# Optimization experiments

Hardware: AMD Instinct MI355X
Metric: run time of the kernel (lower is better)

## Reference

```python
import jax, jax.numpy as jnp
import numpy as np

NUM_HEADS, KEY_DIM, BLOCK, HALO = 8, 64, 8, 4
KV_KERNEL = BLOCK + 2 * HALO  # 16
EMB = NUM_HEADS * KEY_DIM     # 512


def setup_inputs() -> dict:
    key = jax.random.key(0)
    k = jax.random.split(key, 6)
    stddev = KEY_DIM ** -0.5
    return {
        "x": jax.random.normal(k[0], (8, 64, 64, 512), jnp.float32),
        "wq": jax.random.normal(k[1], (512, EMB), jnp.float32) * 0.02,
        "wkv": jax.random.normal(k[2], (512, 2 * EMB), jnp.float32) * 0.02,
        "wout": jax.random.normal(k[3], (EMB, EMB), jnp.float32) * 0.02,
        "pos_w": jax.random.normal(k[4], (KEY_DIM, 2 * KV_KERNEL - 1), jnp.float32) * stddev,
        "pos_h": jax.random.normal(k[5], (KEY_DIM, 2 * KV_KERNEL - 1), jnp.float32) * stddev,
    }


def rel_to_abs(rel):
    # rel: [B, N, hh, ww, 2*pos_dim-1] -> [B, N, hh, ww, pos_dim]
    b, n, hh, ww, dim = rel.shape
    pos_dim = (dim + 1) // 2
    gap = pos_dim - ww
    flat = rel.reshape(b, n, hh, ww * dim)[:, :, :, ww - 1:-1]
    return flat.reshape(b, n, hh, ww, 2 * (pos_dim - 1))[:, :, :, :, gap:pos_dim + gap]


def halo_forward(x, wq, wkv, wout, pos_w, pos_h):
    B, H, W, C = x.shape
    h, w = H // BLOCK, W // BLOCK
    K = KV_KERNEL
    scale = 1.0 / jnp.sqrt(jnp.asarray(KEY_DIM, x.dtype))

    # Query: [B, hd, h, w, block^2, key_dim]
    q = (x @ wq) * scale
    q = q.reshape(B, h, BLOCK, w, BLOCK, NUM_HEADS, KEY_DIM)
    attn_q = q.transpose(0, 5, 1, 3, 2, 4, 6).reshape(B, NUM_HEADS, h, w, BLOCK * BLOCK, KEY_DIM)

    # Overlapping halo KV windows (im2col-style gather, like tf.image.extract_patches)
    kv = x @ wkv
    kv_p = jnp.pad(kv, ((0, 0), (HALO, HALO), (HALO, HALO), (0, 0)))
    idx_h = jnp.arange(h)[:, None] * BLOCK + jnp.arange(K)[None, :]  # [h, K]
    idx_w = jnp.arange(w)[:, None] * BLOCK + jnp.arange(K)[None, :]  # [w, K]
    patches = kv_p[:, idx_h][:, :, :, idx_w]          # [B, h, K, w, K, 2*EMB]
    patches = patches.transpose(0, 1, 3, 2, 4, 5)     # [B, h, w, K, K, 2*EMB]
    patches = patches.reshape(B, h, w, K * K, NUM_HEADS, 2 * KEY_DIM)
    patches = patches.transpose(0, 4, 1, 2, 3, 5)     # [B, hd, h, w, K^2, 2*key_dim]
    key_t, val = patches[..., :KEY_DIM], patches[..., KEY_DIM:]

    scores = jnp.einsum('bnhwqc,bnhwkc->bnhwqk', attn_q, key_t)  # [B,hd,h,w,bq,bk]

    # Relative position logits (width + height), query already carries qk_scale
    pos_q = attn_q.reshape(B, NUM_HEADS * h * w, BLOCK, BLOCK, KEY_DIM)
    rel_w = rel_to_abs(pos_q @ pos_w)                                      # [B,N,hb,wb,K]
    rel_h = rel_to_abs(pos_q.transpose(0, 1, 3, 2, 4) @ pos_h)
    rel_h = rel_h.transpose(0, 1, 3, 2, 4)                                 # [B,N,hb,wb,K]
    pos = rel_w[..., None, :] + rel_h[..., :, None]                        # [B,N,hb,wb,Kh,Kw]
    pos = pos.reshape(B, NUM_HEADS, h, w, BLOCK * BLOCK, K * K)

    attn = jax.nn.softmax(scores + pos, axis=-1)
    out = jnp.einsum('bnhwqk,bnhwkc->bnhwqc', attn, val)
    out = out.reshape(B, NUM_HEADS, h, w, BLOCK, BLOCK, KEY_DIM)
    out = out.transpose(0, 2, 4, 3, 5, 1, 6).reshape(B, H, W, EMB)
    return out @ wout


def reference(x, wq, wkv, wout, pos_w, pos_h):
    return halo_forward(x, wq, wkv, wout, pos_w, pos_h)
```

## Files before the change

### kernel.cpp

```cpp
#include <hip/hip_runtime.h>
#include <hip/hip_fp16.h>
#include <math.h>

typedef _Float16 f16x8 __attribute__((ext_vector_type(8)));
typedef _Float16 f16x4 __attribute__((ext_vector_type(4)));
typedef float    f32x4 __attribute__((ext_vector_type(4)));

#define M_TOT 32768

__device__ __forceinline__ void gload16(const void* g, void* l) {
    __builtin_amdgcn_global_load_lds(
        (const __attribute__((address_space(1))) unsigned int*)g,
        (__attribute__((address_space(3))) unsigned int*)l, 16, 0, 0);
}

__global__ __launch_bounds__(256) void conv_x(const float* __restrict__ x,
                                              __half* __restrict__ y) {
    const size_t i = ((size_t)blockIdx.x * 256 + threadIdx.x) * 8;
    float4 a = *(const float4*)&x[i];
    float4 b = *(const float4*)&x[i + 4];
    __half2 h[4];
    h[0] = __floats2half2_rn(a.x, a.y);
    h[1] = __floats2half2_rn(a.z, a.w);
    h[2] = __floats2half2_rn(b.x, b.y);
    h[3] = __floats2half2_rn(b.z, b.w);
    *(float4*)&y[i] = *(float4*)h;
}

__global__ __launch_bounds__(256) void conv_w(const float* __restrict__ wq,
                                              const float* __restrict__ wkv,
                                              const float* __restrict__ wout,
                                              __half* __restrict__ wT,
                                              __half* __restrict__ woT) {
    const int id = blockIdx.x * 256 + threadIdx.x;
    const int nr = id >> 9, k = id & 511;
    if (nr < 512) {
        wT[(size_t)nr * 512 + k]  = __float2half(wq[k * 512 + nr] * 0.125f);
    } else if (nr < 1536) {
        wT[(size_t)nr * 512 + k]  = __float2half(wkv[k * 1024 + (nr - 512)]);
    } else {
        woT[(size_t)(nr - 1536) * 512 + k] = __float2half(wout[k * 512 + (nr - 1536)]);
    }
}

template <int MODE>
__global__ __launch_bounds__(256) void mfma_gemm(
    const __half* __restrict__ A, const __half* __restrict__ Bt,
    __half* __restrict__ q16, __half* __restrict__ k16, __half* __restrict__ v16,
    float* __restrict__ outf)
{
    __shared__ _Float16 As[128 * 32];
    __shared__ _Float16 Bs[128 * 32];

    const int t = threadIdx.x;
    const int l = t & 63, w = t >> 6;
    const int wr = w >> 1, wc = w & 1;
    const int bm = blockIdx.x, bn = blockIdx.y;

    f32x4 zero = {0.f, 0.f, 0.f, 0.f};
    f32x4 acc[4][4];
    #pragma unroll
    for (int i = 0; i < 4; ++i)
        #pragma unroll
        for (int j = 0; j < 4; ++j) acc[i][j] = zero;

    const int srow = w * 32 + (l >> 2);
    const int sch  = (l & 3) * 8;
    const size_t abase = (size_t)(bm * 128 + srow) * 512 + sch;
    const size_t bbase = (size_t)(bn * 128 + srow) * 512 + sch;
    _Float16* ldsA0 = &As[(w * 2 + 0) * 512];
    _Float16* ldsA1 = &As[(w * 2 + 1) * 512];
    _Float16* ldsB0 = &Bs[(w * 2 + 0) * 512];
    _Float16* ldsB1 = &Bs[(w * 2 + 1) * 512];

    const int lr = l & 15, lk = (l >> 4) * 8;

    for (int k0 = 0; k0 < 512; k0 += 32) {
        gload16(A  + abase + k0,            ldsA0);
        gload16(A  + abase + 16 * 512 + k0, ldsA1);
        gload16(Bt + bbase + k0,            ldsB0);
        gload16(Bt + bbase + 16 * 512 + k0, ldsB1);
        __syncthreads();

        f16x8 af[4], bf[4];
        #pragma unroll
        for (int i = 0; i < 4; ++i)
            af[i] = *(const f16x8*)&As[(wr * 64 + i * 16 + lr) * 32 + lk];
        #pragma unroll
        for (int j = 0; j < 4; ++j)
            bf[j] = *(const f16x8*)&Bs[(wc * 64 + j * 16 + lr) * 32 + lk];
        #pragma unroll
        for (int i = 0; i < 4; ++i)
            #pragma unroll
            for (int j = 0; j < 4; ++j)
                acc[i][j] = __builtin_amdgcn_mfma_f32_16x16x32_f16(af[i], bf[j], acc[i][j], 0, 0, 0);
        __syncthreads();
    }

    const int lq = l >> 4;
    #pragma unroll
    for (int i = 0; i < 4; ++i) {
        #pragma unroll
        for (int j = 0; j < 4; ++j) {
            #pragma unroll
            for (int r = 0; r < 4; ++r) {
                const int row = bm * 128 + wr * 64 + i * 16 + lq * 4 + r;
                const int col = bn * 128 + wc * 64 + j * 16 + lr;
                const float vv = acc[i][j][r];
                if (MODE == 1) {
                    outf[(size_t)row * 512 + col] = vv;
                } else {
                    if (col < 512) {
                        q16[(size_t)row * 512 + col] = __float2half(vv);
                    } else {
                        const int c2 = col - 512;
                        const int head = c2 >> 7, dd = c2 & 127;
                        __half* dst = (dd < 64) ? k16 : v16;
                        dst[(size_t)row * 512 + head * 64 + (dd & 63)] = __float2half(vv);
                    }
                }
            }
        }
    }
}

__global__ __launch_bounds__(256) void transpose_v(const __half* __restrict__ v16,
                                                   __half* __restrict__ vT) {
    __shared__ __half tile[64][72];
    const int wg = blockIdx.x;
    const int tl = wg & 63, n = (wg >> 6) & 7, b = wg >> 9;
    const int px0 = tl * 64;
    const int t = threadIdx.x;

    #pragma unroll
    for (int i = 0; i < 2; ++i) {
        const int c = i * 256 + t;
        const int px = c >> 3, dch = c & 7;
        float4 v = *(const float4*)(v16 + ((size_t)(b * 4096 + px0 + px)) * 512 + n * 64 + dch * 8);
        *(float4*)&tile[px][dch * 8] = v;
    }
    __syncthreads();
    const int d = t & 63, pc = t >> 6;
    __half ov[16];
    #pragma unroll
    for (int j = 0; j < 16; ++j) ov[j] = tile[pc * 16 + j][d];
    __half* dst = vT + ((size_t)((b * 8 + n) * 64 + d)) * 4096 + px0 + pc * 16;
    *(float4*)&dst[0] = *(float4*)&ov[0];
    *(float4*)&dst[8] = *(float4*)&ov[8];
}

__global__ __launch_bounds__(256, 3) void halo_attn(
    const __half* __restrict__ qbuf, const __half* __restrict__ kbuf,
    const __half* __restrict__ vT,
    const float* __restrict__ posw, const float* __restrict__ posh,
    const __half* __restrict__ zp,
    __half* __restrict__ obuf)
{
    __shared__ __align__(16) char KP[64 * 520];
    __shared__ float posq[64][33];
    __shared__ float red[4][64];
    __shared__ float red2[4][64];

    const int hw = blockIdx.x;
    const int wg = (hw & 7) * 512 + (hw >> 3);
    const int wb = wg & 7, hb = (wg >> 3) & 7, n = (wg >> 6) & 7, b = wg >> 9;
    const int t = threadIdx.x;
    const int l = t & 63, g = t >> 6;
    const int hi = l >> 4, c15 = l & 15;

    f16x4 vfrag[16];
    {
        const __half* vrow = vT + ((size_t)((b * 8 + n) * 64 + g * 16 + c15)) * 4096;
        const int x0 = wb * 8 - 4 + hi * 4;
        const bool okx = (unsigned)x0 < 64u;
        #pragma unroll
        for (int kc = 0; kc < 16; ++kc) {
            const int y = hb * 8 - 4 + kc;
            const bool ok = okx && ((unsigned)y < 64u);
            const __half* p = ok ? (vrow + y * 64 + x0) : zp;
            vfrag[kc] = *(const f16x4*)p;
        }
    }

    __half* pwT = (__half*)KP;
    __half* phT = pwT + 31 * 72;
    for (int j5 = t; j5 < 31 * 64; j5 += 256) {
        const int idx = j5 >> 6, d = j5 & 63;
        pwT[idx * 72 + d] = __float2half(posw[d * 31 + idx]);
        phT[idx * 72 + d] = __float2half(posh[d * 31 + idx]);
    }

    const int qrow = l;
    const int pixq = (b * 64 + hb * 8 + (qrow >> 3)) * 64 + wb * 8 + (qrow & 7);
    __half2 qh[32];
    {
        const __half* qsrc = qbuf + (size_t)pixq * 512 + n * 64;
        #pragma unroll
        for (int r = 0; r < 8; ++r) {
            float4 f = *(const float4*)&qsrc[r * 8];
            const __half2* qp = (const __half2*)&f;
            qh[r * 4 + 0] = qp[0]; qh[r * 4 + 1] = qp[1];
            qh[r * 4 + 2] = qp[2]; qh[r * 4 + 3] = qp[3];
        }
    }
    __syncthreads();

    #pragma unroll
    for (int j = 0; j < 8; ++j) {
        const int c = g * 8 + j;
        const int idx = (c < 16) ? (c - (qrow & 7) + 15) : ((c - 16) - (qrow >> 3) + 15);
        const __half* tab = ((c < 16) ? pwT : phT) + idx * 72;
        __half2 a0 = __floats2half2_rn(0.f, 0.f), a1 = a0, a2 = a0, a3 = a0;
        #pragma unroll
        for (int d8 = 0; d8 < 8; ++d8) {
            float4 tv = *(const float4*)&tab[d8 * 8];
            const __half2* tp = (const __half2*)&tv;
            a0 = __hfma2(qh[d8 * 4 + 0], tp[0], a0);
            a1 = __hfma2(qh[d8 * 4 + 1], tp[1], a1);
            a2 = __hfma2(qh[d8 * 4 + 2], tp[2], a2);
            a3 = __hfma2(qh[d8 * 4 + 3], tp[3], a3);
        }
        const __half2 s2 = __hadd2(__hadd2(a0, a1), __hadd2(a2, a3));
        posq[qrow][c] = __low2float(s2) + __high2float(s2);
    }
    __syncthreads();

    #pragma unroll
    for (int it = 0; it < 8; ++it) {
        const int cid = it * 256 + t;
        const int S = cid * 16;
        const int row = S >> 7;
        const int d0h = (((S & 127) >> 4) ^ (row & 7)) * 8;
        const int ky = hb * 8 - 4 + (row >> 4);
        const int kx = wb * 8 - 4 + (row & 15);
        const bool ok = ((unsigned)ky < 64u) && ((unsigned)kx < 64u);
        const __half* src = ok ? (kbuf + ((size_t)((b * 64 + ky) * 64 + kx)) * 512 + n * 64 + d0h)
                               : zp;
        gload16(src, KP + (it * 256 + g * 64) * 16);
    }

    f16x8 qreg[4][2];
    #pragma unroll
    for (int qf = 0; qf < 4; ++qf) {
        const int q = qf * 16 + c15;
        const size_t pix = (size_t)((b * 64 + hb * 8 + (q >> 3)) * 64 + wb * 8 + (q & 7));
        #pragma unroll
        for (int dc = 0; dc < 2; ++dc)
            qreg[qf][dc] = *(const f16x8*)(qbuf + pix * 512 + n * 64 + dc * 32 + hi * 8);
    }
    __syncthreads();

    f32x4 accs[4][4];
    #pragma unroll
    for (int kf = 0; kf < 4; ++kf)
        #pragma unroll
        for (int qf = 0; qf < 4; ++qf) accs[kf][qf] = (f32x4){0.f, 0.f, 0.f, 0.f};

    #pragma unroll
    for (int kf = 0; kf < 4; ++kf) {
        const int row = g * 64 + kf * 16 + c15;
        #pragma unroll
        for (int dc = 0; dc < 2; ++dc) {
            const int off = (row * 128 + dc * 64 + hi * 16) ^ ((row & 7) << 4);
            f16x8 a = *(const f16x8*)(KP + off);
            #pragma unroll
            for (int qf = 0; qf < 4; ++qf)
                accs[kf][qf] = __builtin_amdgcn_mfma_f32_16x16x32_f16(a, qreg[qf][dc], accs[kf][qf], 0, 0, 0);
        }
    }

    float mq[4];
    #pragma unroll
    for (int qf = 0; qf < 4; ++qf) {
        const int q = qf * 16 + c15;
        float pa[4], pb[4];
        #pragma unroll
        for (int r = 0; r < 4; ++r)  pa[r] = posq[q][hi * 4 + r];
        #pragma unroll
        for (int kf = 0; kf < 4; ++kf) pb[kf] = posq[q][16 + g * 4 + kf];
        float mm = -1e30f;
        #pragma unroll
        for (int kf = 0; kf < 4; ++kf)
            #pragma unroll
            for (int r = 0; r < 4; ++r) {
                const float s = accs[kf][qf][r] + pa[r] + pb[kf];
                accs[kf][qf][r] = s;
                mm = fmaxf(mm, s);
            }
        mm = fmaxf(mm, __shfl_xor(mm, 16));
        mm = fmaxf(mm, __shfl_xor(mm, 32));
        mq[qf] = mm;
    }
    if (l < 16) {
        #pragma unroll
        for (int qf = 0; qf < 4; ++qf) red[g][qf * 16 + l] = mq[qf];
    }
    __syncthreads();

    float sums[4];
    #pragma unroll
    for (int qf = 0; qf < 4; ++qf) {
        const int q = qf * 16 + c15;
        const float mfull = fmaxf(fmaxf(red[0][q], red[1][q]), fmaxf(red[2][q], red[3][q]));
        float ss = 0.f;
        #pragma unroll
        for (int kf = 0; kf < 4; ++kf)
            #pragma unroll
            for (int r = 0; r < 4; ++r) {
                const float p = __expf(accs[kf][qf][r] - mfull);
                accs[kf][qf][r] = p;
                ss += p;
            }
        ss += __shfl_xor(ss, 16);
        ss += __shfl_xor(ss, 32);
        sums[qf] = ss;
        #pragma unroll
        for (int kf = 0; kf < 4; ++kf) {
            __half2 h01 = __floats2half2_rn(accs[kf][qf][0], accs[kf][qf][1]);
            __half2 h23 = __floats2half2_rn(accs[kf][qf][2], accs[kf][qf][3]);
            uint2 wv;
            wv.x = *(unsigned*)&h01;
            wv.y = *(unsigned*)&h23;
            *(uint2*)(KP + q * 520 + (g * 64 + kf * 16 + hi * 4) * 2) = wv;
        }
    }
    if (l < 16) {
        #pragma unroll
        for (int qf = 0; qf < 4; ++qf) red2[g][qf * 16 + l] = sums[qf];
    }
    __syncthreads();

    f32x4 acco[4];
    #pragma unroll
    for (int qf = 0; qf < 4; ++qf) acco[qf] = (f32x4){0.f, 0.f, 0.f, 0.f};
    #pragma unroll
    for (int kc = 0; kc < 16; ++kc) {
        const f16x4 bf = vfrag[kc];
        #pragma unroll
        for (int qf = 0; qf < 4; ++qf) {
            const f16x4 af = *(const f16x4*)(KP + (qf * 16 + c15) * 520 + (kc * 16 + hi * 4) * 2);
            acco[qf] = __builtin_amdgcn_mfma_f32_16x16x16f16(af, bf, acco[qf], 0, 0, 0);
        }
    }

    #pragma unroll
    for (int qf = 0; qf < 4; ++qf) {
        #pragma unroll
        for (int r = 0; r < 4; ++r) {
            const int q = qf * 16 + hi * 4 + r;
            const float den = red2[0][q] + red2[1][q] + red2[2][q] + red2[3][q];
            const float v = acco[qf][r] / den;
            const size_t pix = (size_t)((b * 64 + hb * 8 + (q >> 3)) * 64 + wb * 8 + (q & 7));
            obuf[pix * 512 + n * 64 + g * 16 + c15] = __float2half(v);
        }
    }
}

extern "C" void kernel_launch(void* const* d_in, const int* in_sizes, int n_in,
                              void* d_out, int out_size, void* d_ws, size_t ws_size,
                              hipStream_t stream)
{
    const float* x    = (const float*)d_in[0];
    const float* wq   = (const float*)d_in[1];
    const float* wkv  = (const float*)d_in[2];
    const float* wout = (const float*)d_in[3];
    const float* posw = (const float*)d_in[4];
    const float* posh = (const float*)d_in[5];
    float* out = (float*)d_out;

    const size_t NPIX = (size_t)M_TOT * 512;
    __half* x16 = (__half*)d_ws;
    __half* vTb = x16;
    __half* wT  = x16 + NPIX;
    __half* woT = wT + (size_t)1536 * 512;
    __half* q16 = woT + (size_t)512 * 512;
    __half* k16 = q16 + NPIX;
    __half* v16 = k16 + NPIX;
    __half* o16 = v16 + NPIX;
    __half* zp  = o16 + NPIX;

    hipMemsetAsync(zp, 0, 256, stream);

    conv_x<<<(M_TOT * 512) / (256 * 8), 256, 0, stream>>>(x, x16);
    conv_w<<<(2048 * 512) / 256, 256, 0, stream>>>(wq, wkv, wout, wT, woT);

    dim3 g1(M_TOT / 128, 12);
    mfma_gemm<0><<<g1, 256, 0, stream>>>(x16, wT, q16, k16, v16, nullptr);

    transpose_v<<<4096, 256, 0, stream>>>(v16, vTb);

    halo_attn<<<4096, 256, 0, stream>>>(q16, k16, vTb, posw, posh, zp, o16);

    dim3 g3(M_TOT / 128, 4);
    mfma_gemm<1><<<g3, 256, 0, stream>>>(o16, woT, nullptr, nullptr, nullptr, out);
}
```

Baseline: 243.3 us.

## Fuse V transpose into QKV GEMM epilogue and compute rel-pos logits with MFMA

The QKV GEMM epilogue now writes V directly in the transposed [b, head, d, pixel] layout using packed 4-element stores, which removes the separate transpose_v kernel and its extra read and write of V. In the attention kernel, the relative-position logits were computed with scalar half2 FMAs per query. They are now computed as one small MFMA of q against the padded, swizzled pos_w and pos_h tables in LDS, and the result is stored in LDS tables indexed by relative offset. Together these drop one kernel launch and one pass over V, and move the position math onto the matrix cores. In exchange, the transposed V stores are scattered (each store covers only 4 contiguous pixels), and the attention kernel uses more LDS.

After: 227.2 us. -6.6%, faster.

```diff
diff --git a/kernel.cpp b/kernel.cpp
--- a/kernel.cpp
+++ b/kernel.cpp
@@ -46,7 +46,7 @@
 template <int MODE>
 __global__ __launch_bounds__(256) void mfma_gemm(
     const __half* __restrict__ A, const __half* __restrict__ Bt,
-    __half* __restrict__ q16, __half* __restrict__ k16, __half* __restrict__ v16,
+    __half* __restrict__ q16, __half* __restrict__ k16, __half* __restrict__ vT,
     float* __restrict__ outf)
 {
     __shared__ _Float16 As[128 * 32];
@@ -102,51 +102,31 @@
     for (int i = 0; i < 4; ++i) {
         #pragma unroll
         for (int j = 0; j < 4; ++j) {
-            #pragma unroll
-            for (int r = 0; r < 4; ++r) {
-                const int row = bm * 128 + wr * 64 + i * 16 + lq * 4 + r;
-                const int col = bn * 128 + wc * 64 + j * 16 + lr;
-                const float vv = acc[i][j][r];
-                if (MODE == 1) {
-                    outf[(size_t)row * 512 + col] = vv;
-                } else {
-                    if (col < 512) {
-                        q16[(size_t)row * 512 + col] = __float2half(vv);
-                    } else {
-                        const int c2 = col - 512;
-                        const int head = c2 >> 7, dd = c2 & 127;
-                        __half* dst = (dd < 64) ? k16 : v16;
-                        dst[(size_t)row * 512 + head * 64 + (dd & 63)] = __float2half(vv);
-                    }
-                }
+            const int row0 = bm * 128 + wr * 64 + i * 16 + lq * 4;
+            const int col  = bn * 128 + wc * 64 + j * 16 + lr;
+            if (MODE == 1) {
+                #pragma unroll
+                for (int r = 0; r < 4; ++r)
+                    outf[(size_t)(row0 + r) * 512 + col] = acc[i][j][r];
+            } else if (bn < 4) {
+                #pragma unroll
+                for (int r = 0; r < 4; ++r)
+                    q16[(size_t)(row0 + r) * 512 + col] = __float2half(acc[i][j][r]);
+            } else if (wc == 0) {
+                const int head = bn - 4, d2 = j * 16 + lr;
+                #pragma unroll
+                for (int r = 0; r < 4; ++r)
+                    k16[(size_t)(row0 + r) * 512 + head * 64 + d2] = __float2half(acc[i][j][r]);
+            } else {
+                const int head = bn - 4, d2 = j * 16 + lr;
+                const int bb = row0 >> 12, pix = row0 & 4095;
+                f16x4 pv;
+                #pragma unroll
+                for (int r = 0; r < 4; ++r) pv[r] = (_Float16)acc[i][j][r];
+                *(f16x4*)(vT + ((size_t)((bb * 8 + head) * 64 + d2)) * 4096 + pix) = pv;
             }
         }
     }
-}
-
-__global__ __launch_bounds__(256) void transpose_v(const __half* __restrict__ v16,
-                                                   __half* __restrict__ vT) {
-    __shared__ __half tile[64][72];
-    const int wg = blockIdx.x;
-    const int tl = wg & 63, n = (wg >> 6) & 7, b = wg >> 9;
-    const int px0 = tl * 64;
-    const int t = threadIdx.x;
-
-    #pragma unroll
-    for (int i = 0; i < 2; ++i) {
-        const int c = i * 256 + t;
-        const int px = c >> 3, dch = c & 7;
-        float4 v = *(const float4*)(v16 + ((size_t)(b * 4096 + px0 + px)) * 512 + n * 64 + dch * 8);
-        *(float4*)&tile[px][dch * 8] = v;
-    }
-    __syncthreads();
-    const int d = t & 63, pc = t >> 6;
-    __half ov[16];
-    #pragma unroll
-    for (int j = 0; j < 16; ++j) ov[j] = tile[pc * 16 + j][d];
-    __half* dst = vT + ((size_t)((b * 8 + n) * 64 + d)) * 4096 + px0 + pc * 16;
-    *(float4*)&dst[0] = *(float4*)&ov[0];
-    *(float4*)&dst[8] = *(float4*)&ov[8];
 }
 
 __global__ __launch_bounds__(256, 3) void halo_attn(
@@ -157,7 +137,8 @@
     __half* __restrict__ obuf)
 {
     __shared__ __align__(16) char KP[64 * 520];
-    __shared__ float posq[64][33];
+    __shared__ float RWT[32][68];
+    __shared__ float RHT[32][68];
     __shared__ float red[4][64];
     __shared__ float red2[4][64];
 
@@ -182,46 +163,39 @@
         }
     }
 
-    __half* pwT = (__half*)KP;
-    __half* phT = pwT + 31 * 72;
-    for (int j5 = t; j5 < 31 * 64; j5 += 256) {
-        const int idx = j5 >> 6, d = j5 & 63;
-        pwT[idx * 72 + d] = __float2half(posw[d * 31 + idx]);
-        phT[idx * 72 + d] = __float2half(posh[d * 31 + idx]);
-    }
-
-    const int qrow = l;
-    const int pixq = (b * 64 + hb * 8 + (qrow >> 3)) * 64 + wb * 8 + (qrow & 7);
-    __half2 qh[32];
+    for (int j5 = t; j5 < 4096; j5 += 256) {
+        const int tb = j5 >> 11, idx = (j5 >> 6) & 31, d = j5 & 63;
+        const float* src = tb ? posh : posw;
+        const float v = (idx < 31) ? src[d * 31 + idx] : 0.f;
+        *(__half*)(KP + tb * 4096 + ((idx * 128 + d * 2) ^ ((idx & 7) << 4))) = __float2half(v);
+    }
+
+    f16x8 qreg[4][2];
+    #pragma unroll
+    for (int qf = 0; qf < 4; ++qf) {
+        const int q = qf * 16 + c15;
+        const size_t pix = (size_t)((b * 64 + hb * 8 + (q >> 3)) * 64 + wb * 8 + (q & 7));
+        #pragma unroll
+        for (int dc = 0; dc < 2; ++dc)
+            qreg[qf][dc] = *(const f16x8*)(qbuf + pix * 512 + n * 64 + dc * 32 + hi * 8);
+    }
+    __syncthreads();
+
+    f32x4 accp[4];
+    #pragma unroll
+    for (int qf = 0; qf < 4; ++qf) accp[qf] = (f32x4){0.f, 0.f, 0.f, 0.f};
     {
-        const __half* qsrc = qbuf + (size_t)pixq * 512 + n * 64;
-        #pragma unroll
-        for (int r = 0; r < 8; ++r) {
-            float4 f = *(const float4*)&qsrc[r * 8];
-            const __half2* qp = (const __half2*)&f;
-            qh[r * 4 + 0] = qp[0]; qh[r * 4 + 1] = qp[1];
-            qh[r * 4 + 2] = qp[2]; qh[r * 4 + 3] = qp[3];
-        }
-    }
-    __syncthreads();
-
-    #pragma unroll
-    for (int j = 0; j < 8; ++j) {
-        const int c = g * 8 + j;
-        const int idx = (c < 16) ? (c - (qrow & 7) + 15) : ((c - 16) - (qrow >> 3) + 15);
-        const __half* tab = ((c < 16) ? pwT : phT) + idx * 72;
-        __half2 a0 = __floats2half2_rn(0.f, 0.f), a1 = a0, a2 = a0, a3 = a0;
-        #pragma unroll
-        for (int d8 = 0; d8 < 8; ++d8) {
-            float4 tv = *(const float4*)&tab[d8 * 8];
-            const __half2* tp = (const __half2*)&tv;
-            a0 = __hfma2(qh[d8 * 4 + 0], tp[0], a0);
-            a1 = __hfma2(qh[d8 * 4 + 1], tp[1], a1);
-            a2 = __hfma2(qh[d8 * 4 + 2], tp[2], a2);
-            a3 = __hfma2(qh[d8 * 4 + 3], tp[3], a3);
-        }
-        const __half2 s2 = __hadd2(__hadd2(a0, a1), __hadd2(a2, a3));
-        posq[qrow][c] = __low2float(s2) + __high2float(s2);
+        const int tb = g >> 1, ih = g & 1;
+        const char* base = KP + tb * 4096;
+        const int row = ih * 16 + c15;
+        #pragma unroll
+        for (int dc = 0; dc < 2; ++dc) {
+            const int off = (row * 128 + dc * 64 + hi * 16) ^ ((row & 7) << 4);
+            f16x8 a = *(const f16x8*)(base + off);
+            #pragma unroll
+            for (int qf = 0; qf < 4; ++qf)
+                accp[qf] = __builtin_amdgcn_mfma_f32_16x16x32_f16(a, qreg[qf][dc], accp[qf], 0, 0, 0);
+        }
     }
     __syncthreads();
 
@@ -239,14 +213,14 @@
         gload16(src, KP + (it * 256 + g * 64) * 16);
     }
 
-    f16x8 qreg[4][2];
-    #pragma unroll
-    for (int qf = 0; qf < 4; ++qf) {
-        const int q = qf * 16 + c15;
-        const size_t pix = (size_t)((b * 64 + hb * 8 + (q >> 3)) * 64 + wb * 8 + (q & 7));
-        #pragma unroll
-        for (int dc = 0; dc < 2; ++dc)
-            qreg[qf][dc] = *(const f16x8*)(qbuf + pix * 512 + n * 64 + dc * 32 + hi * 8);
+    {
+        const int tb = g >> 1, ih = g & 1;
+        float (*dst)[68] = tb ? RHT : RWT;
+        #pragma unroll
+        for (int qf = 0; qf < 4; ++qf)
+            #pragma unroll
+            for (int r = 0; r < 4; ++r)
+                dst[ih * 16 + hi * 4 + r][qf * 16 + c15] = accp[qf][r];
     }
     __syncthreads();
 
@@ -273,11 +247,12 @@
     #pragma unroll
     for (int qf = 0; qf < 4; ++qf) {
         const int q = qf * 16 + c15;
+        const int qj = q & 7, qi = q >> 3;
         float pa[4], pb[4];
         #pragma unroll
-        for (int r = 0; r < 4; ++r)  pa[r] = posq[q][hi * 4 + r];
-        #pragma unroll
-        for (int kf = 0; kf < 4; ++kf) pb[kf] = posq[q][16 + g * 4 + kf];
+        for (int r = 0; r < 4; ++r)  pa[r] = RWT[hi * 4 + r - qj + 15][q];
+        #pragma unroll
+        for (int kf = 0; kf < 4; ++kf) pb[kf] = RHT[g * 4 + kf - qi + 15][q];
         float mm = -1e30f;
         #pragma unroll
         for (int kf = 0; kf < 4; ++kf)
@@ -370,13 +345,12 @@
 
     const size_t NPIX = (size_t)M_TOT * 512;
     __half* x16 = (__half*)d_ws;
-    __half* vTb = x16;
     __half* wT  = x16 + NPIX;
     __half* woT = wT + (size_t)1536 * 512;
     __half* q16 = woT + (size_t)512 * 512;
     __half* k16 = q16 + NPIX;
-    __half* v16 = k16 + NPIX;
-    __half* o16 = v16 + NPIX;
+    __half* vT  = k16 + NPIX;
+    __half* o16 = vT + NPIX;
     __half* zp  = o16 + NPIX;
 
     hipMemsetAsync(zp, 0, 256, stream);
@@ -385,11 +359,9 @@
     conv_w<<<(2048 * 512) / 256, 256, 0, stream>>>(wq, wkv, wout, wT, woT);
 
     dim3 g1(M_TOT / 128, 12);
-    mfma_gemm<0><<<g1, 256, 0, stream>>>(x16, wT, q16, k16, v16, nullptr);
-
-    transpose_v<<<4096, 256, 0, stream>>>(v16, vTb);
-
-    halo_attn<<<4096, 256, 0, stream>>>(q16, k16, vTb, posw, posh, zp, o16);
+    mfma_gemm<0><<<g1, 256, 0, stream>>>(x16, wT, q16, k16, vT, nullptr);
+
+    halo_attn<<<4096, 256, 0, stream>>>(q16, k16, vT, posw, posh, zp, o16);
 
     dim3 g3(M_TOT / 128, 4);
     mfma_gemm<1><<<g3, 256, 0, stream>>>(o16, woT, nullptr, nullptr, nullptr, out);
```
